# Kernel optimization log

Measured on AMD Instinct MI355X. Metric: run time of the kernel, lower is better.

The kernel has to match this reference:

```python
import jax, jax.numpy as jnp
import numpy as np

NUM_HEADS = 8
CH_PER_HEAD = 32
NUM_GROUPS = 32
EPS = 1e-5
SCALE = CH_PER_HEAD ** (-0.25)


def setup_inputs() -> dict:
    key = jax.random.key(0)
    ks = jax.random.split(key, 6)
    B, C, H, W = 2, 256, 64, 64
    hid = NUM_HEADS * CH_PER_HEAD  # 256
    s = 1.0 / np.sqrt(C)
    return {
        "x": jax.random.normal(ks[0], (B, C, H, W), dtype=jnp.float32),
        "gamma": jnp.ones((C,), jnp.float32),
        "beta": jnp.zeros((C,), jnp.float32),
        "wq": jax.random.normal(ks[1], (hid, C), jnp.float32) * s,
        "bq": jnp.zeros((hid,), jnp.float32),
        "wk": jax.random.normal(ks[2], (hid, C), jnp.float32) * s,
        "bk": jnp.zeros((hid,), jnp.float32),
        "wv": jax.random.normal(ks[3], (hid, C), jnp.float32) * s,
        "bv": jnp.zeros((hid,), jnp.float32),
        "wout": jax.random.normal(ks[4], (C, hid), jnp.float32) * s,
        "bout": jnp.zeros((C,), jnp.float32),
    }


def _group_norm(x, gamma, beta):
    b, c, h, w = x.shape
    xg = x.reshape(b, NUM_GROUPS, c // NUM_GROUPS, h, w)
    mu = jnp.mean(xg, axis=(2, 3, 4), keepdims=True)
    var = jnp.var(xg, axis=(2, 3, 4), keepdims=True)
    xg = (xg - mu) * jax.lax.rsqrt(var + EPS)
    return xg.reshape(b, c, h, w) * gamma[None, :, None, None] + beta[None, :, None, None]


def reference(x, gamma, beta, wq, bq, wk, bk, wv, bv, wout, bout):
    b, c, h, w = x.shape
    n = h * w
    x_n = _group_norm(x, gamma, beta).reshape(b, c, n)  # b c n (self-attention: embedding = x_n)
    # 1x1 convs == pointwise linear over the channel dim
    q = jnp.einsum('oc,bcn->bon', wq, x_n) + bq[None, :, None]
    k = jnp.einsum('oc,bcn->bon', wk, x_n) + bk[None, :, None]
    v = jnp.einsum('oc,bcn->bon', wv, x_n) + bv[None, :, None]
    # split heads: b (h d) n -> b h d n
    d = CH_PER_HEAD
    q = q.reshape(b, NUM_HEADS, d, n)
    k = k.reshape(b, NUM_HEADS, d, n)
    v = v.reshape(b, NUM_HEADS, d, n)
    attn = jax.nn.softmax(jnp.einsum('bhdi,bhdj->bhij', q * SCALE, k * SCALE), axis=-1)
    out = jnp.einsum('bhij,bhdj->bhdi', attn, v).reshape(b, NUM_HEADS * d, n)
    out = jnp.einsum('oc,bcn->bon', wout, out) + bout[None, :, None]
    out = out.reshape(b, -1, h, w)
    return x + out  # shapes match -> residual
```

## Files before the change

### kernel.cpp

```cpp
#include <hip/hip_runtime.h>
#include <hip/hip_bf16.h>
#include <stdint.h>

typedef unsigned short u16;
typedef float f32x4 __attribute__((ext_vector_type(4)));
typedef float f32x16 __attribute__((ext_vector_type(16)));
typedef short bf16x8 __attribute__((ext_vector_type(8)));

#define NSP 4096
#define CDIM 256
#define HID 256
#define NH 8
#define DH 32
#define NG 32
#define CPG 8
#define BATCH 2
#define SPLIT 4
#define GN_EPS 1e-5f
#define QK2_SCALE 0.25503488f

#define MFMA32(A, B, C) __builtin_amdgcn_mfma_f32_32x32x16_bf16(A, B, C, 0, 0, 0)
#define MFMA16(A, B, C) __builtin_amdgcn_mfma_f32_16x16x32_bf16(A, B, C, 0, 0, 0)

__device__ __forceinline__ float bf2f(u16 u) {
    union { uint32_t i; float f; } v; v.i = ((uint32_t)u) << 16; return v.f;
}
__device__ __forceinline__ u16 f2bf(float f) {
    union { float f; uint32_t i; } v; v.f = f;
    uint32_t b = v.i;
    return (u16)((b + 0x7FFFu + ((b >> 16) & 1u)) >> 16);
}

__device__ __forceinline__ void gload16(const u16* g, u16* lds) {
    __builtin_amdgcn_global_load_lds(
        (const __attribute__((address_space(1))) uint32_t*)g,
        (__attribute__((address_space(3))) uint32_t*)lds, 16, 0, 0);
}

__device__ __forceinline__ void pl32swap(uint32_t& a, uint32_t& b) {
    asm("v_permlane32_swap_b32 %0, %1" : "+v"(a), "+v"(b));
}

__global__ void gn_stats(const float* __restrict__ x, float* __restrict__ stats,
                         const float* __restrict__ wq, const float* __restrict__ wk,
                         const float* __restrict__ wv, const float* __restrict__ wout,
                         u16* __restrict__ wcat) {
    int blk = blockIdx.x;
#pragma unroll
    for (int i = 0; i < 16; i++) {
        int idx = blk * 4096 + i * 256 + threadIdx.x;
        const float* src = (idx < 65536) ? wq : (idx < 131072) ? wk : (idx < 196608) ? wv : wout;
        wcat[idx] = f2bf(src[idx & 65535]);
    }
    const float4* base = (const float4*)(x + (size_t)blk * (CPG * NSP));
    float s = 0.f, ss = 0.f;
    for (int i = threadIdx.x; i < (CPG * NSP) / 4; i += 256) {
        float4 v = base[i];
        s  += v.x + v.y + v.z + v.w;
        ss += v.x * v.x + v.y * v.y + v.z * v.z + v.w * v.w;
    }
    for (int m = 1; m < 64; m <<= 1) { s += __shfl_xor(s, m, 64); ss += __shfl_xor(ss, m, 64); }
    __shared__ float ls[4], lss[4];
    int w = threadIdx.x >> 6;
    if ((threadIdx.x & 63) == 0) { ls[w] = s; lss[w] = ss; }
    __syncthreads();
    if (threadIdx.x == 0) {
        float S = ls[0] + ls[1] + ls[2] + ls[3];
        float SS = lss[0] + lss[1] + lss[2] + lss[3];
        float mean = S / (float)(CPG * NSP);
        float var = SS / (float)(CPG * NSP) - mean * mean;
        stats[2 * blk] = mean;
        stats[2 * blk + 1] = rsqrtf(var + GN_EPS);
    }
}

__global__ void gn_apply(const float* __restrict__ x, const float* __restrict__ stats,
                         const float* __restrict__ gamma, const float* __restrict__ beta,
                         u16* __restrict__ xn) {
    __shared__ u16 tile[64][72];
    int n0 = blockIdx.x * 64, c0 = blockIdx.y * 64, b = blockIdx.z;
    int t = threadIdx.x;
    int nl = t & 63, cq = t >> 6;
#pragma unroll
    for (int i = 0; i < 16; i++) {
        int cl = i * 4 + cq;
        int c = c0 + cl;
        int g = c >> 3;
        float mean = stats[2 * (b * NG + g)];
        float rstd = stats[2 * (b * NG + g) + 1];
        float v = x[((size_t)b * CDIM + c) * NSP + n0 + nl];
        v = (v - mean) * rstd * gamma[c] + beta[c];
        tile[cl][nl] = f2bf(v);
    }
    __syncthreads();
    int nr = t >> 2, cc = (t & 3) * 16;
    uint4 o0, o1;
    u16* p0 = (u16*)&o0; u16* p1 = (u16*)&o1;
#pragma unroll
    for (int j = 0; j < 8; j++) { p0[j] = tile[cc + j][nr]; p1[j] = tile[cc + 8 + j][nr]; }
    size_t orow = ((size_t)b * NSP + n0 + nr) * CDIM + c0 + cc;
    *(uint4*)(xn + orow) = o0;
    *(uint4*)(xn + orow + 8) = o1;
}

__global__ __launch_bounds__(256) void gemm_qkv(
    const u16* __restrict__ A, const u16* __restrict__ wcat,
    const float* __restrict__ bq, const float* __restrict__ bk, const float* __restrict__ bv,
    u16* __restrict__ qb, u16* __restrict__ kfb, u16* __restrict__ vfb) {
    __shared__ u16 As[128 * 64];
    __shared__ u16 Bs[128 * 64];
    int bz = blockIdx.z;
    const u16* Ab = A + (size_t)bz * NSP * CDIM;
    int n0 = blockIdx.x * 128, m0 = blockIdx.y * 128;
    int seg = n0 >> 8;
    int t = threadIdx.x, lane = t & 63, w = t >> 6;
    int wr = w >> 1, wc = w & 1;
    f32x4 acc[4][4] = {};

    int srow = w * 8 + (lane >> 3);
    int scol = (lane & 7) * 8;
    const u16* asrc = Ab + (size_t)(m0 + srow) * CDIM + scol;
    const u16* bsrc = wcat + (size_t)(n0 + srow) * CDIM + scol;
    u16* albase = As + w * 512;
    u16* blbase = Bs + w * 512;

    int frow = lane & 15, fcol = (lane >> 4) * 8;

    for (int k0 = 0; k0 < CDIM; k0 += 64) {
        __syncthreads();
#pragma unroll
        for (int ro = 0; ro < 4; ro++) {
            gload16(asrc + (size_t)ro * 32 * CDIM + k0, albase + ro * 2048);
            gload16(bsrc + (size_t)ro * 32 * CDIM + k0, blbase + ro * 2048);
        }
        asm volatile("s_waitcnt vmcnt(0)" ::: "memory");
        __syncthreads();
#pragma unroll
        for (int kk = 0; kk < 2; kk++) {
            bf16x8 af[4], bfv[4];
#pragma unroll
            for (int i = 0; i < 4; i++) {
                af[i]  = *(bf16x8*)&As[(wr * 64 + i * 16 + frow) * 64 + kk * 32 + fcol];
                bfv[i] = *(bf16x8*)&Bs[(wc * 64 + i * 16 + frow) * 64 + kk * 32 + fcol];
            }
#pragma unroll
            for (int i = 0; i < 4; i++)
#pragma unroll
                for (int j = 0; j < 4; j++)
                    acc[i][j] = MFMA16(af[i], bfv[j], acc[i][j]);
        }
    }

    const float* bias = (seg == 0) ? bq : (seg == 1) ? bk : bv;
    int r4 = (lane >> 4) * 4, cx = lane & 15;
#pragma unroll
    for (int i = 0; i < 4; i++) {
        int rbase = m0 + wr * 64 + i * 16 + r4;
#pragma unroll
        for (int j = 0; j < 4; j++) {
            int col = n0 + wc * 64 + j * 16 + cx;
            int cb = col & 255;
            float bb = bias[cb];
            if (seg == 0) {
#pragma unroll
                for (int r = 0; r < 4; r++)
                    qb[(size_t)bz * NSP * HID + (size_t)(rbase + r) * HID + cb] = f2bf(acc[i][j][r] + bb);
            } else if (seg == 1) {
                int h2 = cb >> 5;
                int f = 2 * ((rbase >> 5) & 1) + ((cb >> 4) & 1);
                size_t kt = ((size_t)(bz * NH + h2) * 64 + (rbase >> 6)) * 2048
                          + (size_t)f * 512 + ((rbase & 31) + (((cb >> 3) & 1) << 5)) * 8 + (cb & 7);
#pragma unroll
                for (int r = 0; r < 4; r++)
                    kfb[kt + r * 8] = f2bf((acc[i][j][r] + bb) * QK2_SCALE);
            } else {
                int h2 = cb >> 5, d = cb & 31;
                int jc = (rbase >> 3) & 7;
                size_t vt = ((size_t)(bz * NH + h2) * 64 + (rbase >> 6)) * 2048
                          + (size_t)(jc >> 1) * 512 + (d + ((jc & 1) << 5)) * 8 + (rbase & 7);
                uint2 pkd;
                pkd.x = ((uint32_t)f2bf(acc[i][j][1] + bb) << 16) | f2bf(acc[i][j][0] + bb);
                pkd.y = ((uint32_t)f2bf(acc[i][j][3] + bb) << 16) | f2bf(acc[i][j][2] + bb);
                *(uint2*)(vfb + vt) = pkd;
            }
        }
    }
}

__global__ __launch_bounds__(256) void gemm_out(
    const u16* __restrict__ A,
    const u16* __restrict__ B, long sB,
    const float* __restrict__ bias,
    const float* __restrict__ resid, long sR,
    float* __restrict__ outp, long sO,
    int N) {
    __shared__ u16 As[64][72];
    __shared__ u16 Bs[64][72];
    int bz = blockIdx.z;
    B += (size_t)bz * sB;
    int m0 = blockIdx.y * 64, n0 = blockIdx.x * 64;
    int t = threadIdx.x, lane = t & 63, w = t >> 6;
    int wm = (w >> 1) * 32, wn = (w & 1) * 32;
    f32x4 acc[2][2] = {};

    int sr = t >> 2;
    int sc1 = (t & 3) * 8, sc2 = sc1 + 32;

    uint4 av0 = *(const uint4*)(A + (size_t)(m0 + sr) * CDIM + sc1);
    uint4 av1 = *(const uint4*)(A + (size_t)(m0 + sr) * CDIM + sc2);
    uint4 bv0 = *(const uint4*)(B + (size_t)(n0 + sr) * CDIM + sc1);
    uint4 bv1 = *(const uint4*)(B + (size_t)(n0 + sr) * CDIM + sc2);

    for (int k0 = 0; k0 < CDIM; k0 += 64) {
        __syncthreads();
        *(uint4*)&As[sr][sc1] = av0;
        *(uint4*)&As[sr][sc2] = av1;
        *(uint4*)&Bs[sr][sc1] = bv0;
        *(uint4*)&Bs[sr][sc2] = bv1;
        __syncthreads();
        if (k0 + 64 < CDIM) {
            av0 = *(const uint4*)(A + (size_t)(m0 + sr) * CDIM + k0 + 64 + sc1);
            av1 = *(const uint4*)(A + (size_t)(m0 + sr) * CDIM + k0 + 64 + sc2);
            bv0 = *(const uint4*)(B + (size_t)(n0 + sr) * CDIM + k0 + 64 + sc1);
            bv1 = *(const uint4*)(B + (size_t)(n0 + sr) * CDIM + k0 + 64 + sc2);
        }
#pragma unroll
        for (int ks = 0; ks < 2; ks++) {
            bf16x8 af[2], bfr[2];
#pragma unroll
            for (int i = 0; i < 2; i++) {
                af[i]  = *(bf16x8*)&As[wm + i * 16 + (lane & 15)][ks * 32 + (lane >> 4) * 8];
                bfr[i] = *(bf16x8*)&Bs[wn + i * 16 + (lane & 15)][ks * 32 + (lane >> 4) * 8];
            }
#pragma unroll
            for (int i = 0; i < 2; i++)
#pragma unroll
                for (int j = 0; j < 2; j++)
                    acc[i][j] = MFMA16(af[i], bfr[j], acc[i][j]);
        }
    }

    int r4 = (lane >> 4) * 4, cx = lane & 15;
#pragma unroll
    for (int i = 0; i < 2; i++)
#pragma unroll
        for (int j = 0; j < 2; j++) {
            int rbase = m0 + wm + i * 16 + r4;
            int cbase = n0 + wn + j * 16 + cx;
#pragma unroll
            for (int r = 0; r < 4; r++) {
                int row = rbase + r, col = cbase;
                outp[(size_t)bz * sO + (size_t)row * N + col] =
                    acc[i][j][r] + bias[row] + resid[(size_t)bz * sR + (size_t)row * N + col];
            }
        }
}

__global__ __launch_bounds__(256, 2) void attn_kernel(
    const u16* __restrict__ q, const u16* __restrict__ kfb,
    const u16* __restrict__ vfb, u16* __restrict__ po, float* __restrict__ zz) {
    int h = blockIdx.y;
    int bz = blockIdx.z;
    int b = bz >> 2, sp = bz & 3;
    int kv0 = sp * (NSP / SPLIT);
    int t = threadIdx.x, lane = t & 63, w = t >> 6;
    int ql = lane & 31, hi = lane >> 5;
    int q0 = blockIdx.x * 256 + w * 64;

    const u16* qbp = q + (size_t)b * NSP * HID + (size_t)(q0 + ql) * HID + h * DH + hi * 8;
    bf16x8 qa0 = *(const bf16x8*)(qbp);
    bf16x8 qa1 = *(const bf16x8*)(qbp + 16);
    bf16x8 qb0 = *(const bf16x8*)(qbp + 32 * HID);
    bf16x8 qb1 = *(const bf16x8*)(qbp + 32 * HID + 16);

    size_t tbase = ((size_t)(b * NH + h) * 64 + (kv0 >> 6)) * 2048 + (size_t)lane * 8;
    const u16* kp = kfb + tbase;
    const u16* vp = vfb + tbase;

#define LOADT(kd, vd, it) { \
    kd[0] = *(const bf16x8*)(kp + (size_t)(it) * 2048);        \
    kd[1] = *(const bf16x8*)(kp + (size_t)(it) * 2048 + 512);  \
    kd[2] = *(const bf16x8*)(kp + (size_t)(it) * 2048 + 1024); \
    kd[3] = *(const bf16x8*)(kp + (size_t)(it) * 2048 + 1536); \
    vd[0] = *(const bf16x8*)(vp + (size_t)(it) * 2048);        \
    vd[1] = *(const bf16x8*)(vp + (size_t)(it) * 2048 + 512);  \
    vd[2] = *(const bf16x8*)(vp + (size_t)(it) * 2048 + 1024); \
    vd[3] = *(const bf16x8*)(vp + (size_t)(it) * 2048 + 1536); }

    union { uint32_t u[4]; bf16x8 v8; } ones;
    ones.u[0] = 0x3F803F80u; ones.u[1] = 0x3F803F80u;
    ones.u[2] = 0x3F803F80u; ones.u[3] = 0x3F803F80u;

    f32x16 kzero = {};
    f32x16 oacc_a = {}, oacc_b = {};
    f32x16 lsum_a = {}, lsum_b = {};

    auto softpv = [&](f32x16& st, const bf16x8 (&vf)[4], int tt, f32x16& oacc, f32x16& lsum) {
        uint32_t pk[8];
#pragma unroll
        for (int j = 0; j < 8; j++) {
            float p0 = __builtin_amdgcn_exp2f(st[2 * j]);
            float p1 = __builtin_amdgcn_exp2f(st[2 * j + 1]);
            uint32_t dd;
            asm("v_cvt_pk_bf16_f32 %0, %1, %2" : "=v"(dd) : "v"(p0), "v"(p1));
            pk[j] = dd;
        }
#pragma unroll
        for (int c = 0; c < 2; c++) {
            uint32_t a0 = pk[4 * c + 0], b0 = pk[4 * c + 2];
            uint32_t a1 = pk[4 * c + 1], b1 = pk[4 * c + 3];
            pl32swap(a0, b0);
            pl32swap(a1, b1);
            union { uint32_t u[4]; bf16x8 v8; } fr;
            fr.u[0] = a0; fr.u[1] = a1; fr.u[2] = b0; fr.u[3] = b1;
            __builtin_amdgcn_s_setprio(1);
            oacc = MFMA32(fr.v8, vf[2 * tt + c], oacc);
            lsum = MFMA32(fr.v8, ones.v8, lsum);
            __builtin_amdgcn_s_setprio(0);
        }
    };

    auto process = [&](const bf16x8 (&kf)[4], const bf16x8 (&vf)[4]) {
#pragma unroll
        for (int tt = 0; tt < 2; tt++) {
            __builtin_amdgcn_s_setprio(1);
            f32x16 st_a = MFMA32(kf[2 * tt], qa0, kzero);
            st_a = MFMA32(kf[2 * tt + 1], qa1, st_a);
            f32x16 st_b = MFMA32(kf[2 * tt], qb0, kzero);
            st_b = MFMA32(kf[2 * tt + 1], qb1, st_b);
            __builtin_amdgcn_s_setprio(0);
            softpv(st_a, vf, tt, oacc_a, lsum_a);
            softpv(st_b, vf, tt, oacc_b, lsum_b);
        }
    };

    const int NT = (NSP / SPLIT) / 64;
    bf16x8 ka[4], va[4], kc[4], vc[4];
    LOADT(ka, va, 0);
    for (int it = 0; it < NT; it += 2) {
        int n1 = (it + 1 < NT) ? it + 1 : 0;
        LOADT(kc, vc, n1);
        process(ka, va);
        int n2 = (it + 2 < NT) ? it + 2 : 0;
        LOADT(ka, va, n2);
        process(kc, vc);
    }
#undef LOADT

    float* zrow = zz + (((size_t)bz * NH + h) * NSP) + q0;
    if (ql == 0) {
#pragma unroll
        for (int r = 0; r < 16; r++) {
            int qq = (r & 3) + 8 * (r >> 2) + 4 * hi;
            zrow[qq] = __log2f(lsum_a[r]);
            zrow[32 + qq] = __log2f(lsum_b[r]);
        }
    }
    u16* pob = po + ((((size_t)bz * NH + h) * NSP) + q0) * DH + ql;
#pragma unroll
    for (int r = 0; r < 16; r++) {
        int qq = (r & 3) + 8 * (r >> 2) + 4 * hi;
        pob[(size_t)qq * DH] = f2bf(oacc_a[r] / lsum_a[r]);
        pob[(size_t)(32 + qq) * DH] = f2bf(oacc_b[r] / lsum_b[r]);
    }
}

__global__ __launch_bounds__(256) void combine_kernel(
    const u16* __restrict__ po, const float* __restrict__ zz, u16* __restrict__ ao) {
    int idx = blockIdx.x * 256 + threadIdx.x;
    int c8 = idx & 31;
    int n  = (idx >> 5) & (NSP - 1);
    int b  = idx >> 17;
    int h  = c8 >> 2;
    int dp = (c8 & 3) * 8;

    float z[SPLIT];
    size_t base[SPLIT];
    float M = -3e38f;
#pragma unroll
    for (int s = 0; s < SPLIT; s++) {
        base[s] = ((((size_t)(b * SPLIT + s) * NH + h) * NSP) + n);
        z[s] = zz[base[s]];
        M = fmaxf(M, z[s]);
    }
    float wsum = 0.f, acc[8] = {};
#pragma unroll
    for (int s = 0; s < SPLIT; s++) {
        float ww = __builtin_amdgcn_exp2f(z[s] - M);
        wsum += ww;
        uint4 o = *(const uint4*)(po + base[s] * DH + dp);
        const u16* op = (const u16*)&o;
#pragma unroll
        for (int j = 0; j < 8; j++) acc[j] += bf2f(op[j]) * ww;
    }
    float inv = 1.0f / wsum;
    uint4 r;
    u16* rp = (u16*)&r;
#pragma unroll
    for (int j = 0; j < 8; j++) rp[j] = f2bf(acc[j] * inv);
    *(uint4*)(ao + (((size_t)b * NSP + n) * HID) + h * DH + dp) = r;
}

extern "C" void kernel_launch(void* const* d_in, const int* in_sizes, int n_in,
                              void* d_out, int out_size, void* d_ws, size_t ws_size,
                              hipStream_t stream) {
    const float* x     = (const float*)d_in[0];
    const float* gamma = (const float*)d_in[1];
    const float* beta  = (const float*)d_in[2];
    const float* wq    = (const float*)d_in[3];
    const float* bq    = (const float*)d_in[4];
    const float* wk    = (const float*)d_in[5];
    const float* bk    = (const float*)d_in[6];
    const float* wv    = (const float*)d_in[7];
    const float* bv    = (const float*)d_in[8];
    const float* wout  = (const float*)d_in[9];
    const float* bout  = (const float*)d_in[10];
    float* out = (float*)d_out;

    char* ws = (char*)d_ws;
    float* stats = (float*)ws;
    u16* wq_b = (u16*)(ws + 4096);
    u16* wo_b = wq_b + 3 * 65536;
    u16* xn = wo_b + 65536;
    u16* qb = xn + (size_t)BATCH * NSP * CDIM;
    u16* kfb = qb + (size_t)BATCH * NSP * HID;
    u16* vfb = kfb + (size_t)BATCH * NH * 64 * 2048;
    u16* aob = vfb + (size_t)BATCH * NH * 64 * 2048;
    u16* pob = aob + (size_t)BATCH * NSP * HID;
    float* zzb = (float*)(pob + (size_t)SPLIT * BATCH * NH * NSP * DH);

    const long sQ = (long)NSP * HID;
    const long sOut = (long)CDIM * NSP;

    gn_stats<<<BATCH * NG, 256, 0, stream>>>(x, stats, wq, wk, wv, wout, wq_b);
    gn_apply<<<dim3(NSP / 64, CDIM / 64, BATCH), 256, 0, stream>>>(x, stats, gamma, beta, xn);

    gemm_qkv<<<dim3(768 / 128, NSP / 128, BATCH), 256, 0, stream>>>(
        xn, wq_b, bq, bk, bv, qb, kfb, vfb);

    attn_kernel<<<dim3(NSP / 256, NH, BATCH * SPLIT), 256, 0, stream>>>(qb, kfb, vfb, pob, zzb);
    combine_kernel<<<(BATCH * NSP * HID / 8) / 256, 256, 0, stream>>>(pob, zzb, aob);

    gemm_out<<<dim3(NSP / 64, CDIM / 64, BATCH), 256, 0, stream>>>(
        wo_b, aob, sQ, bout, x, sOut, out, sOut, NSP);
}
```

Before: 93.84 us.

## Halve queries per wave, compute softmax row sums on VALU, raise attention occupancy

Each wave in the attention kernel now handles 32 queries instead of 64, so each block covers 128 queries and the grid is twice as large. The launch bound now targets 4 blocks per CU. Softmax row sums are now accumulated with scalar adds plus a cross-half shuffle, replacing the extra MFMA against a ones vector; this cuts matrix work on the P·V path. V loads are issued per tile, and normalization uses a wave-local LDS table of reciprocals. The cost is that every K/V tile is loaded for half as many queries, roughly doubling K/V read traffic from cache.

```diff
diff --git a/kernel.cpp b/kernel.cpp
--- a/kernel.cpp
+++ b/kernel.cpp
@@ -256,112 +256,98 @@
         }
 }
 
-__global__ __launch_bounds__(256, 2) void attn_kernel(
+__global__ __launch_bounds__(256, 4) void attn_kernel(
     const u16* __restrict__ q, const u16* __restrict__ kfb,
     const u16* __restrict__ vfb, u16* __restrict__ po, float* __restrict__ zz) {
+    __shared__ float Ls[4][32];
     int h = blockIdx.y;
     int bz = blockIdx.z;
     int b = bz >> 2, sp = bz & 3;
     int kv0 = sp * (NSP / SPLIT);
     int t = threadIdx.x, lane = t & 63, w = t >> 6;
     int ql = lane & 31, hi = lane >> 5;
-    int q0 = blockIdx.x * 256 + w * 64;
+    int q0 = blockIdx.x * 128 + w * 32;
 
     const u16* qbp = q + (size_t)b * NSP * HID + (size_t)(q0 + ql) * HID + h * DH + hi * 8;
-    bf16x8 qa0 = *(const bf16x8*)(qbp);
-    bf16x8 qa1 = *(const bf16x8*)(qbp + 16);
-    bf16x8 qb0 = *(const bf16x8*)(qbp + 32 * HID);
-    bf16x8 qb1 = *(const bf16x8*)(qbp + 32 * HID + 16);
+    bf16x8 qf0 = *(const bf16x8*)(qbp);
+    bf16x8 qf1 = *(const bf16x8*)(qbp + 16);
 
     size_t tbase = ((size_t)(b * NH + h) * 64 + (kv0 >> 6)) * 2048 + (size_t)lane * 8;
     const u16* kp = kfb + tbase;
     const u16* vp = vfb + tbase;
 
-#define LOADT(kd, vd, it) { \
+#define LOADKF(kd, it) { \
     kd[0] = *(const bf16x8*)(kp + (size_t)(it) * 2048);        \
     kd[1] = *(const bf16x8*)(kp + (size_t)(it) * 2048 + 512);  \
     kd[2] = *(const bf16x8*)(kp + (size_t)(it) * 2048 + 1024); \
-    kd[3] = *(const bf16x8*)(kp + (size_t)(it) * 2048 + 1536); \
+    kd[3] = *(const bf16x8*)(kp + (size_t)(it) * 2048 + 1536); }
+#define LOADVF(vd, it) { \
     vd[0] = *(const bf16x8*)(vp + (size_t)(it) * 2048);        \
     vd[1] = *(const bf16x8*)(vp + (size_t)(it) * 2048 + 512);  \
     vd[2] = *(const bf16x8*)(vp + (size_t)(it) * 2048 + 1024); \
     vd[3] = *(const bf16x8*)(vp + (size_t)(it) * 2048 + 1536); }
 
-    union { uint32_t u[4]; bf16x8 v8; } ones;
-    ones.u[0] = 0x3F803F80u; ones.u[1] = 0x3F803F80u;
-    ones.u[2] = 0x3F803F80u; ones.u[3] = 0x3F803F80u;
-
     f32x16 kzero = {};
-    f32x16 oacc_a = {}, oacc_b = {};
-    f32x16 lsum_a = {}, lsum_b = {};
-
-    auto softpv = [&](f32x16& st, const bf16x8 (&vf)[4], int tt, f32x16& oacc, f32x16& lsum) {
-        uint32_t pk[8];
-#pragma unroll
-        for (int j = 0; j < 8; j++) {
-            float p0 = __builtin_amdgcn_exp2f(st[2 * j]);
-            float p1 = __builtin_amdgcn_exp2f(st[2 * j + 1]);
-            uint32_t dd;
-            asm("v_cvt_pk_bf16_f32 %0, %1, %2" : "=v"(dd) : "v"(p0), "v"(p1));
-            pk[j] = dd;
-        }
-#pragma unroll
-        for (int c = 0; c < 2; c++) {
-            uint32_t a0 = pk[4 * c + 0], b0 = pk[4 * c + 2];
-            uint32_t a1 = pk[4 * c + 1], b1 = pk[4 * c + 3];
-            pl32swap(a0, b0);
-            pl32swap(a1, b1);
-            union { uint32_t u[4]; bf16x8 v8; } fr;
-            fr.u[0] = a0; fr.u[1] = a1; fr.u[2] = b0; fr.u[3] = b1;
-            __builtin_amdgcn_s_setprio(1);
-            oacc = MFMA32(fr.v8, vf[2 * tt + c], oacc);
-            lsum = MFMA32(fr.v8, ones.v8, lsum);
-            __builtin_amdgcn_s_setprio(0);
-        }
-    };
+    f32x16 oacc = {};
+    float l0 = 0.f, l1 = 0.f;
 
     auto process = [&](const bf16x8 (&kf)[4], const bf16x8 (&vf)[4]) {
 #pragma unroll
         for (int tt = 0; tt < 2; tt++) {
             __builtin_amdgcn_s_setprio(1);
-            f32x16 st_a = MFMA32(kf[2 * tt], qa0, kzero);
-            st_a = MFMA32(kf[2 * tt + 1], qa1, st_a);
-            f32x16 st_b = MFMA32(kf[2 * tt], qb0, kzero);
-            st_b = MFMA32(kf[2 * tt + 1], qb1, st_b);
+            f32x16 st = MFMA32(kf[2 * tt], qf0, kzero);
+            st = MFMA32(kf[2 * tt + 1], qf1, st);
             __builtin_amdgcn_s_setprio(0);
-            softpv(st_a, vf, tt, oacc_a, lsum_a);
-            softpv(st_b, vf, tt, oacc_b, lsum_b);
+            uint32_t pk[8];
+#pragma unroll
+            for (int j = 0; j < 8; j++) {
+                float p0 = __builtin_amdgcn_exp2f(st[2 * j]);
+                float p1 = __builtin_amdgcn_exp2f(st[2 * j + 1]);
+                float ps = p0 + p1;
+                if (j & 1) l1 += ps; else l0 += ps;
+                uint32_t dd;
+                asm("v_cvt_pk_bf16_f32 %0, %1, %2" : "=v"(dd) : "v"(p0), "v"(p1));
+                pk[j] = dd;
+            }
+#pragma unroll
+            for (int c = 0; c < 2; c++) {
+                uint32_t a0 = pk[4 * c + 0], b0 = pk[4 * c + 2];
+                uint32_t a1 = pk[4 * c + 1], b1 = pk[4 * c + 3];
+                pl32swap(a0, b0);
+                pl32swap(a1, b1);
+                union { uint32_t u[4]; bf16x8 v8; } fr;
+                fr.u[0] = a0; fr.u[1] = a1; fr.u[2] = b0; fr.u[3] = b1;
+                __builtin_amdgcn_s_setprio(1);
+                oacc = MFMA32(fr.v8, vf[2 * tt + c], oacc);
+                __builtin_amdgcn_s_setprio(0);
+            }
         }
     };
 
     const int NT = (NSP / SPLIT) / 64;
-    bf16x8 ka[4], va[4], kc[4], vc[4];
-    LOADT(ka, va, 0);
+    bf16x8 ka[4], kc[4], va[4];
+    LOADKF(ka, 0);
     for (int it = 0; it < NT; it += 2) {
-        int n1 = (it + 1 < NT) ? it + 1 : 0;
-        LOADT(kc, vc, n1);
+        LOADVF(va, it);
+        LOADKF(kc, it + 1);
         process(ka, va);
+        LOADVF(va, it + 1);
         int n2 = (it + 2 < NT) ? it + 2 : 0;
-        LOADT(ka, va, n2);
-        process(kc, vc);
-    }
-#undef LOADT
-
-    float* zrow = zz + (((size_t)bz * NH + h) * NSP) + q0;
-    if (ql == 0) {
-#pragma unroll
-        for (int r = 0; r < 16; r++) {
-            int qq = (r & 3) + 8 * (r >> 2) + 4 * hi;
-            zrow[qq] = __log2f(lsum_a[r]);
-            zrow[32 + qq] = __log2f(lsum_b[r]);
-        }
-    }
+        LOADKF(ka, n2);
+        process(kc, va);
+    }
+#undef LOADKF
+#undef LOADVF
+
+    float l = l0 + l1;
+    l += __shfl_xor(l, 32);
+    Ls[w][ql] = 1.0f / l;
+    if (hi == 0) zz[(((size_t)bz * NH + h) * NSP) + q0 + ql] = __log2f(l);
     u16* pob = po + ((((size_t)bz * NH + h) * NSP) + q0) * DH + ql;
 #pragma unroll
     for (int r = 0; r < 16; r++) {
         int qq = (r & 3) + 8 * (r >> 2) + 4 * hi;
-        pob[(size_t)qq * DH] = f2bf(oacc_a[r] / lsum_a[r]);
-        pob[(size_t)(32 + qq) * DH] = f2bf(oacc_b[r] / lsum_b[r]);
+        pob[(size_t)qq * DH] = f2bf(oacc[r] * Ls[w][qq]);
     }
 }
 
@@ -438,7 +424,7 @@
     gemm_qkv<<<dim3(768 / 128, NSP / 128, BATCH), 256, 0, stream>>>(
         xn, wq_b, bq, bk, bv, qb, kfb, vfb);
 
-    attn_kernel<<<dim3(NSP / 256, NH, BATCH * SPLIT), 256, 0, stream>>>(qb, kfb, vfb, pob, zzb);
+    attn_kernel<<<dim3(NSP / 128, NH, BATCH * SPLIT), 256, 0, stream>>>(qb, kfb, vfb, pob, zzb);
     combine_kernel<<<(BATCH * NSP * HID / 8) / 256, 256, 0, stream>>>(pob, zzb, aob);
 
     gemm_out<<<dim3(NSP / 64, CDIM / 64, BATCH), 256, 0, stream>>>(
```

New measurement: 93.42 us. Within noise of the previous version (-0.4%).
